# Performance work log

Measured on AMD Instinct MI355X. Metric: run time of the kernel, lower is better.

The kernel has to match this reference:

```python
import jax, jax.numpy as jnp
import numpy as np

D = 1024
H = 16
DK = D // H
FF = int(8 / 3 * D)  # 2730
EPS = 1e-6


def setup_inputs() -> dict:
    key = jax.random.key(0)
    ks = jax.random.split(key, 8)
    s = lambda n: 1.0 / np.sqrt(n)
    return {
        "x": jax.random.normal(ks[0], (2, 2048, D), dtype=jnp.float32),
        "w_qkv": jax.random.normal(ks[1], (3 * D, D), dtype=jnp.float32) * s(D),
        "w_o": jax.random.normal(ks[2], (D, D), dtype=jnp.float32) * s(D),
        "n1_w": jnp.ones((D,), dtype=jnp.float32),
        "n2_w": jnp.ones((D,), dtype=jnp.float32),
        "w1": jax.random.normal(ks[3], (FF, D), dtype=jnp.float32) * s(D),
        "w2": jax.random.normal(ks[4], (D, FF), dtype=jnp.float32) * s(FF),
        "w3": jax.random.normal(ks[5], (FF, D), dtype=jnp.float32) * s(D),
    }


def _rmsnorm(x, w):
    return x * jax.lax.rsqrt(jnp.mean(x * x, axis=-1, keepdims=True) + EPS) * w


def _attn(x, w_qkv, w_o):
    B, L, _ = x.shape
    qkv = x @ w_qkv.T                       # [B,L,3D]
    qkv = qkv.reshape(B, L, 3, H, DK)
    q, k, v = qkv[:, :, 0], qkv[:, :, 1], qkv[:, :, 2]   # [B,L,H,DK]
    scores = jnp.einsum("blhd,bmhd->bhlm", q, k) / np.sqrt(DK).astype(np.float32)
    attn = jax.nn.softmax(scores, axis=-1)               # [B,H,L,L]
    out = jnp.einsum("bhlm,bmhd->blhd", attn, v).reshape(B, L, D)
    return out @ w_o.T


def _swiglu(x, w1, w2, w3):
    return (jax.nn.silu(x @ w1.T) * (x @ w3.T)) @ w2.T


def reference(x, w_qkv, w_o, n1_w, n2_w, w1, w2, w3):
    x = x + _attn(_rmsnorm(x, n1_w), w_qkv, w_o)
    return x + _swiglu(_rmsnorm(x, n2_w), w1, w2, w3)
```

## Files before the change

kernel.cpp:

```cpp
#include <hip/hip_runtime.h>
#include <stdint.h>


#define LSEQ   2048
#define DMODEL 1024
#define NHEAD  16
#define NTOK   4096
#define FFR    2730
#define FFP    2816
#define FF2    5632

typedef short  short8  __attribute__((ext_vector_type(8)));
typedef float  floatx4 __attribute__((ext_vector_type(4)));

__device__ __forceinline__ uint16_t f2bf(float f) {
  uint32_t u = __builtin_bit_cast(uint32_t, f);
  u += 0x7FFFu + ((u >> 16) & 1u);
  return (uint16_t)(u >> 16);
}
__device__ __forceinline__ float bf2f(uint16_t s) {
  uint32_t u = ((uint32_t)s) << 16;
  return __builtin_bit_cast(float, u);
}
__device__ __forceinline__ void gl2lds16(const void* g, void* l) {
  __builtin_amdgcn_global_load_lds(
      (const __attribute__((address_space(1))) unsigned int*)g,
      (__attribute__((address_space(3))) unsigned int*)l, 16, 0, 0);
}

__global__ __launch_bounds__(256) void cvt_all_k(const float* __restrict__ wqkv,
                                                 const float* __restrict__ wo,
                                                 const float* __restrict__ w1,
                                                 const float* __restrict__ w3,
                                                 uint16_t* __restrict__ dst) {
  int g = blockIdx.x;
  int c = threadIdx.x * 4;
  const float* src = nullptr;
  if (g < 3072)       src = wqkv + (size_t)g * 1024;
  else if (g < 4096)  src = wo + (size_t)(g - 3072) * 1024;
  else {
    int r = g - 4096;
    int u = r >> 6, wi = r & 63;
    int srow = u * 32 + (wi & 31);
    if (srow < FFR) src = ((wi < 32) ? w1 : w3) + (size_t)srow * 1024;
  }
  float4 v = src ? *(const float4*)(src + c) : float4{0, 0, 0, 0};
  uint64_t pack =  (uint64_t)f2bf(v.x)        | ((uint64_t)f2bf(v.y) << 16)
                | ((uint64_t)f2bf(v.z) << 32) | ((uint64_t)f2bf(v.w) << 48);
  *(uint64_t*)(dst + (size_t)g * 1024 + c) = pack;
}

__global__ void cvt_pad_k(const float* __restrict__ src, uint16_t* __restrict__ dst,
                          int rows, int cols, int cols_p, long total) {
  long idx = (long)blockIdx.x * 256 + threadIdx.x;
  if (idx >= total) return;
  int r = (int)(idx / cols_p);
  int c = (int)(idx % cols_p);
  float v = (r < rows && c < cols) ? src[(size_t)r * cols + c] : 0.0f;
  dst[idx] = f2bf(v);
}

__global__ __launch_bounds__(256) void rmsnorm_k(const float* __restrict__ x,
                                                 const float* __restrict__ wgt,
                                                 uint16_t* __restrict__ out) {
  const int row = blockIdx.x;
  const int c = threadIdx.x * 4;
  const float* xr = x + (size_t)row * DMODEL;
  float4 v = *(const float4*)(xr + c);
  float ss = v.x * v.x + v.y * v.y + v.z * v.z + v.w * v.w;
#pragma unroll
  for (int off = 32; off >= 1; off >>= 1) ss += __shfl_down(ss, off, 64);
  __shared__ float red[4];
  if ((threadIdx.x & 63) == 0) red[threadIdx.x >> 6] = ss;
  __syncthreads();
  float tot = red[0] + red[1] + red[2] + red[3];
  float scale = rsqrtf(tot * (1.0f / DMODEL) + 1e-6f);
  float4 wv = *(const float4*)(wgt + c);
  uint64_t pack =  (uint64_t)f2bf(v.x * scale * wv.x)
                | ((uint64_t)f2bf(v.y * scale * wv.y) << 16)
                | ((uint64_t)f2bf(v.z * scale * wv.z) << 32)
                | ((uint64_t)f2bf(v.w * scale * wv.w) << 48);
  *(uint64_t*)(out + (size_t)row * DMODEL + c) = pack;
}

template <int MODE, int TM, int TN>
__global__ __launch_bounds__(256) void gemm_bt(const uint16_t* __restrict__ A,
                                               const uint16_t* __restrict__ B,
                                               uint16_t* __restrict__ Cb,
                                               float* __restrict__ Cf,
                                               const float* __restrict__ Res,
                                               int M, int N, int K) {
  constexpr int FI = TM / 32, FJ = TN / 32;
  constexpr int NIT = (TM + TN) / 64;
  __shared__ uint16_t As[TM * 32];
  __shared__ uint16_t Bs[TN * 32];
  const int tid = threadIdx.x;
  const int w = tid >> 6, lane = tid & 63;
  const int grp = lane >> 4, l16 = lane & 15;
  const int m0 = blockIdx.y * TM, n0 = blockIdx.x * TN;
  const int rw = (w >> 1) * (TM / 2), cw = (w & 1) * (TN / 2);

  floatx4 acc[FI][FJ] = {};

  const uint16_t* gp[NIT];
  uint16_t* lp[NIT];
#pragma unroll
  for (int i = 0; i < NIT; i++) {
    int c = i * 256 + tid;
    if (c < TM * 4) {
      gp[i] = A + (size_t)(m0 + (c >> 2)) * K + (c & 3) * 8;
      lp[i] = As + c * 8;
    } else {
      int c2 = c - TM * 4;
      gp[i] = B + (size_t)(n0 + (c2 >> 2)) * K + (c2 & 3) * 8;
      lp[i] = Bs + c2 * 8;
    }
  }

  for (int k0 = 0; k0 < K; k0 += 32) {
#pragma unroll
    for (int i = 0; i < NIT; i++) gl2lds16(gp[i] + k0, lp[i]);
    __syncthreads();
    short8 af[FI], bfr[FJ];
#pragma unroll
    for (int i = 0; i < FI; i++)
      af[i] = *(const short8*)(As + (rw + i * 16 + l16) * 32 + grp * 8);
#pragma unroll
    for (int j = 0; j < FJ; j++)
      bfr[j] = *(const short8*)(Bs + (cw + j * 16 + l16) * 32 + grp * 8);
#pragma unroll
    for (int i = 0; i < FI; i++)
#pragma unroll
      for (int j = 0; j < FJ; j++)
        acc[i][j] = __builtin_amdgcn_mfma_f32_16x16x32_bf16(af[i], bfr[j], acc[i][j], 0, 0, 0);
    __syncthreads();
  }

  if constexpr (MODE == 2) {
    const int half = N >> 1;
#pragma unroll
    for (int i = 0; i < FI; i++) {
      const int mrow = m0 + rw + i * 16 + grp * 4;
#pragma unroll
      for (int j = 0; j < 2; j++) {
        const int gcol = (n0 >> 1) + (cw >> 1) + j * 16 + l16;
#pragma unroll
        for (int r = 0; r < 4; r++) {
          float a = acc[i][j][r];
          float bv = acc[i][j + 2][r];
          float ex = __builtin_amdgcn_exp2f(-a * 1.4426950408889634f);
          float s = a * __builtin_amdgcn_rcpf(1.0f + ex);
          Cb[(size_t)(mrow + r) * half + gcol] = f2bf(s * bv);
        }
      }
    }
  } else {
#pragma unroll
    for (int i = 0; i < FI; i++) {
#pragma unroll
      for (int j = 0; j < FJ; j++) {
        const int mrow = m0 + rw + i * 16 + grp * 4;
        const int ncol = n0 + cw + j * 16 + l16;
#pragma unroll
        for (int r = 0; r < 4; r++) {
          size_t idx = (size_t)(mrow + r) * N + ncol;
          float v = acc[i][j][r];
          if (MODE == 0) Cb[idx] = f2bf(v);
          else           Cf[idx] = v + Res[idx];
        }
      }
    }
  }
}

__global__ __launch_bounds__(256) void attn_flash(const uint16_t* __restrict__ qkv,
                                                  uint16_t* __restrict__ outp) {
  const int tid = threadIdx.x;
  const int w = tid >> 6, lane = tid & 63;
  const int grp = lane >> 4, l16 = lane & 15;
  const int lin = blockIdx.x;
  const int xcd = lin & 7;
  const int slot = lin >> 3;
  const int pair = xcd * 4 + (slot >> 4);
  const int qc = slot & 15;
  const int h = pair & 15, b = pair >> 4;
  const int q0 = qc * 128;

  __shared__ uint16_t Qs[8192];
  __shared__ uint16_t Ks[2][4096];
  __shared__ uint16_t Vt[2][64 * 76];
  __shared__ uint16_t Ps[128 * 76];

  const size_t base = ((size_t)b * LSEQ) * 3072 + (size_t)h * 64;

#pragma unroll
  for (int i = 0; i < 4; i++) {
    int c = i * 256 + tid;
    int row = c >> 3, cc = (c & 7) ^ (row & 7);
    gl2lds16(qkv + base + (size_t)(q0 + row) * 3072 + cc * 8, Qs + c * 8);
  }
#pragma unroll
  for (int i = 0; i < 2; i++) {
    int c = i * 256 + tid;
    int row = c >> 3, cc = (c & 7) ^ (row & 7);
    gl2lds16(qkv + base + (size_t)row * 3072 + 1024 + cc * 8, Ks[0] + c * 8);
  }
#pragma unroll
  for (int i = 0; i < 2; i++) {
    int c = i * 256 + tid;
    int tt = c & 63, db = c >> 6;
    uint4 vv = *(const uint4*)(qkv + base + (size_t)tt * 3072 + 2048 + db * 8);
    uint32_t uu[4] = {vv.x, vv.y, vv.z, vv.w};
#pragma unroll
    for (int e = 0; e < 4; e++) {
      Vt[0][(db * 8 + e * 2 + 0) * 76 + tt] = (uint16_t)(uu[e] & 0xFFFFu);
      Vt[0][(db * 8 + e * 2 + 1) * 76 + tt] = (uint16_t)(uu[e] >> 16);
    }
  }
  __syncthreads();

  short8 aq[2][2];
#pragma unroll
  for (int fi = 0; fi < 2; fi++) {
    const int qrow = w * 32 + fi * 16 + l16;
#pragma unroll
    for (int kk = 0; kk < 2; kk++) {
      int cc = kk * 4 + grp;
      aq[fi][kk] = *(const short8*)(Qs + (qrow * 8 + (cc ^ (qrow & 7))) * 8);
    }
  }

  float lsum[2][4] = {};
  floatx4 o_acc[2][4] = {};
  const float C = 0.125f * 1.4426950408889634f;

  for (int kc = 0; kc < LSEQ / 64; kc++) {
    const int cur = kc & 1, nxt = cur ^ 1;
    const bool pre = (kc + 1 < LSEQ / 64);
    const int t1 = (kc + 1) * 64;
    uint4 vv[2];
    if (pre) {
#pragma unroll
      for (int i = 0; i < 2; i++) {
        int c = i * 256 + tid;
        int row = c >> 3, cc = (c & 7) ^ (row & 7);
        gl2lds16(qkv + base + (size_t)(t1 + row) * 3072 + 1024 + cc * 8, Ks[nxt] + c * 8);
      }
#pragma unroll
      for (int i = 0; i < 2; i++) {
        int c = i * 256 + tid;
        int tt = c & 63, db = c >> 6;
        vv[i] = *(const uint4*)(qkv + base + (size_t)(t1 + tt) * 3072 + 2048 + db * 8);
      }
    }

    floatx4 s_acc[2][4] = {};
#pragma unroll
    for (int j = 0; j < 4; j++) {
      const int krow = j * 16 + l16;
#pragma unroll
      for (int kk = 0; kk < 2; kk++) {
        int cc = kk * 4 + grp;
        short8 bk = *(const short8*)(Ks[cur] + (krow * 8 + (cc ^ (krow & 7))) * 8);
#pragma unroll
        for (int fi = 0; fi < 2; fi++)
          s_acc[fi][j] = __builtin_amdgcn_mfma_f32_16x16x32_bf16(aq[fi][kk], bk, s_acc[fi][j], 0, 0, 0);
      }
    }

#pragma unroll
    for (int fi = 0; fi < 2; fi++) {
      const int prow = w * 32 + fi * 16 + grp * 4;
#pragma unroll
      for (int j = 0; j < 4; j++)
#pragma unroll
        for (int r = 0; r < 4; r++) {
          float pv = __builtin_amdgcn_exp2f(s_acc[fi][j][r] * C);
          lsum[fi][r] += pv;
          Ps[(prow + r) * 76 + j * 16 + l16] = f2bf(pv);
        }
    }

#pragma unroll
    for (int kk = 0; kk < 2; kk++) {
      short8 ap0 = *(const short8*)(Ps + (w * 32 + l16) * 76 + kk * 32 + grp * 8);
      short8 ap1 = *(const short8*)(Ps + (w * 32 + 16 + l16) * 76 + kk * 32 + grp * 8);
#pragma unroll
      for (int jj = 0; jj < 4; jj++) {
        short8 bv = *(const short8*)(Vt[cur] + (jj * 16 + l16) * 76 + kk * 32 + grp * 8);
        o_acc[0][jj] = __builtin_amdgcn_mfma_f32_16x16x32_bf16(ap0, bv, o_acc[0][jj], 0, 0, 0);
        o_acc[1][jj] = __builtin_amdgcn_mfma_f32_16x16x32_bf16(ap1, bv, o_acc[1][jj], 0, 0, 0);
      }
    }

    if (pre) {
#pragma unroll
      for (int i = 0; i < 2; i++) {
        int c = i * 256 + tid;
        int tt = c & 63, db = c >> 6;
        uint32_t uu[4] = {vv[i].x, vv[i].y, vv[i].z, vv[i].w};
#pragma unroll
        for (int e = 0; e < 4; e++) {
          Vt[nxt][(db * 8 + e * 2 + 0) * 76 + tt] = (uint16_t)(uu[e] & 0xFFFFu);
          Vt[nxt][(db * 8 + e * 2 + 1) * 76 + tt] = (uint16_t)(uu[e] >> 16);
        }
      }
    }
    __syncthreads();
  }

#pragma unroll
  for (int off = 8; off >= 1; off >>= 1)
#pragma unroll
    for (int fi = 0; fi < 2; fi++)
#pragma unroll
      for (int r = 0; r < 4; r++) lsum[fi][r] += __shfl_xor(lsum[fi][r], off, 64);
#pragma unroll
  for (int fi = 0; fi < 2; fi++)
#pragma unroll
    for (int jj = 0; jj < 4; jj++)
#pragma unroll
      for (int r = 0; r < 4; r++) {
        int row = b * LSEQ + q0 + w * 32 + fi * 16 + grp * 4 + r;
        float o = o_acc[fi][jj][r] * __builtin_amdgcn_rcpf(lsum[fi][r]);
        outp[(size_t)row * DMODEL + h * 64 + jj * 16 + l16] = f2bf(o);
      }
}

extern "C" void kernel_launch(void* const* d_in, const int* in_sizes, int n_in,
                              void* d_out, int out_size, void* d_ws, size_t ws_size,
                              hipStream_t stream) {
  const float* x    = (const float*)d_in[0];
  const float* wqkv = (const float*)d_in[1];
  const float* wo   = (const float*)d_in[2];
  const float* n1w  = (const float*)d_in[3];
  const float* n2w  = (const float*)d_in[4];
  const float* w1   = (const float*)d_in[5];
  const float* w2   = (const float*)d_in[6];
  const float* w3   = (const float*)d_in[7];
  float* out = (float*)d_out;

  char* p = (char*)d_ws;
  uint16_t* wall  = (uint16_t*)p; p += (size_t)9728 * 1024 * 2;
  uint16_t* wqkvb = wall;
  uint16_t* wob   = wall + (size_t)3072 * 1024;
  uint16_t* w13b  = wall + (size_t)4096 * 1024;
  uint16_t* w2b   = (uint16_t*)p; p += (size_t)1024 * FFP * 2;
  uint16_t* h1    = (uint16_t*)p; p += (size_t)NTOK * DMODEL * 2;
  uint16_t* qkvb  = (uint16_t*)p; p += (size_t)NTOK * 3072 * 2;
  uint16_t* attno = (uint16_t*)p; p += (size_t)NTOK * DMODEL * 2;
  float*    x1    = (float*)p;    p += (size_t)NTOK * DMODEL * 4;
  uint16_t* h2    = (uint16_t*)p; p += (size_t)NTOK * DMODEL * 2;
  uint16_t* gbuf  = (uint16_t*)p; p += (size_t)NTOK * FFP * 2;

  cvt_all_k<<<9728, 256, 0, stream>>>(wqkv, wo, w1, w3, wall);
  cvt_pad_k<<<(1024 * FFP) / 256, 256, 0, stream>>>(w2, w2b, 1024, FFR, FFP, 1024L * FFP);

  rmsnorm_k<<<NTOK, 256, 0, stream>>>(x, n1w, h1);
  gemm_bt<0, 128, 128><<<dim3(3072 / 128, NTOK / 128), 256, 0, stream>>>(
      h1, wqkvb, qkvb, nullptr, nullptr, NTOK, 3072, 1024);
  attn_flash<<<512, 256, 0, stream>>>(qkvb, attno);
  gemm_bt<1, 128, 64><<<dim3(1024 / 64, NTOK / 128), 256, 0, stream>>>(
      attno, wob, nullptr, x1, x, NTOK, 1024, 1024);
  rmsnorm_k<<<NTOK, 256, 0, stream>>>(x1, n2w, h2);
  gemm_bt<2, 128, 128><<<dim3(FF2 / 128, NTOK / 128), 256, 0, stream>>>(
      h2, w13b, gbuf, nullptr, nullptr, NTOK, FF2, 1024);
  gemm_bt<1, 128, 64><<<dim3(1024 / 64, NTOK / 128), 256, 0, stream>>>(
      gbuf, w2b, nullptr, out, x1, NTOK, 1024, FFP);
}
```

Before: 390.7 us.

## Halve attention query tile, compute transposed scores, use packed bf16 conversion

The attention kernel now handles 64 query rows per block instead of 128 and launches 1024 blocks, so each wave owns 16 query rows. It computes S^T (K as the A operand) so each lane holds a contiguous row fragment of P and can write packed bf16 pairs. Q and P share one LDS buffer and the row-sum reduction goes through LDS, which cuts LDS use and should raise occupancy. The convert and rmsnorm kernels use the hardware v_cvt_pk_bf16_f32 instruction instead of software rounding. Smaller tiles mean K/V are read from global memory twice as often per query, and the padded strides change the LDS bank-conflict pattern.

```diff
diff --git a/kernel.cpp b/kernel.cpp
--- a/kernel.cpp
+++ b/kernel.cpp
@@ -10,6 +10,9 @@
 #define FFP    2816
 #define FF2    5632
 
+#define PSTR   72
+#define VSTR   70
+
 typedef short  short8  __attribute__((ext_vector_type(8)));
 typedef float  floatx4 __attribute__((ext_vector_type(4)));
 
@@ -21,6 +24,11 @@
 __device__ __forceinline__ float bf2f(uint16_t s) {
   uint32_t u = ((uint32_t)s) << 16;
   return __builtin_bit_cast(float, u);
+}
+__device__ __forceinline__ uint32_t pk_bf16(float a, float b) {
+  uint32_t d;
+  asm("v_cvt_pk_bf16_f32 %0, %1, %2" : "=v"(d) : "v"(a), "v"(b));
+  return d;
 }
 __device__ __forceinline__ void gl2lds16(const void* g, void* l) {
   __builtin_amdgcn_global_load_lds(
@@ -45,9 +53,8 @@
     if (srow < FFR) src = ((wi < 32) ? w1 : w3) + (size_t)srow * 1024;
   }
   float4 v = src ? *(const float4*)(src + c) : float4{0, 0, 0, 0};
-  uint64_t pack =  (uint64_t)f2bf(v.x)        | ((uint64_t)f2bf(v.y) << 16)
-                | ((uint64_t)f2bf(v.z) << 32) | ((uint64_t)f2bf(v.w) << 48);
-  *(uint64_t*)(dst + (size_t)g * 1024 + c) = pack;
+  uint2 pk = {pk_bf16(v.x, v.y), pk_bf16(v.z, v.w)};
+  *(uint2*)(dst + (size_t)g * 1024 + c) = pk;
 }
 
 __global__ void cvt_pad_k(const float* __restrict__ src, uint16_t* __restrict__ dst,
@@ -76,11 +83,9 @@
   float tot = red[0] + red[1] + red[2] + red[3];
   float scale = rsqrtf(tot * (1.0f / DMODEL) + 1e-6f);
   float4 wv = *(const float4*)(wgt + c);
-  uint64_t pack =  (uint64_t)f2bf(v.x * scale * wv.x)
-                | ((uint64_t)f2bf(v.y * scale * wv.y) << 16)
-                | ((uint64_t)f2bf(v.z * scale * wv.z) << 32)
-                | ((uint64_t)f2bf(v.w * scale * wv.w) << 48);
-  *(uint64_t*)(out + (size_t)row * DMODEL + c) = pack;
+  uint2 pk = {pk_bf16(v.x * scale * wv.x, v.y * scale * wv.y),
+              pk_bf16(v.z * scale * wv.z, v.w * scale * wv.w)};
+  *(uint2*)(out + (size_t)row * DMODEL + c) = pk;
 }
 
 template <int MODE, int TM, int TN>
@@ -181,20 +186,21 @@
   const int lin = blockIdx.x;
   const int xcd = lin & 7;
   const int slot = lin >> 3;
-  const int pair = xcd * 4 + (slot >> 4);
-  const int qc = slot & 15;
+  const int pair = xcd * 4 + (slot >> 5);
+  const int qc = slot & 31;
   const int h = pair & 15, b = pair >> 4;
-  const int q0 = qc * 128;
-
-  __shared__ uint16_t Qs[8192];
+  const int q0 = qc * 64;
+
+  __shared__ uint16_t QP[64 * PSTR];
   __shared__ uint16_t Ks[2][4096];
-  __shared__ uint16_t Vt[2][64 * 76];
-  __shared__ uint16_t Ps[128 * 76];
+  __shared__ uint16_t Vt[2][64 * VSTR];
+  uint16_t* Qs = QP;
+  uint16_t* Ps = QP;
 
   const size_t base = ((size_t)b * LSEQ) * 3072 + (size_t)h * 64;
 
 #pragma unroll
-  for (int i = 0; i < 4; i++) {
+  for (int i = 0; i < 2; i++) {
     int c = i * 256 + tid;
     int row = c >> 3, cc = (c & 7) ^ (row & 7);
     gl2lds16(qkv + base + (size_t)(q0 + row) * 3072 + cc * 8, Qs + c * 8);
@@ -213,25 +219,25 @@
     uint32_t uu[4] = {vv.x, vv.y, vv.z, vv.w};
 #pragma unroll
     for (int e = 0; e < 4; e++) {
-      Vt[0][(db * 8 + e * 2 + 0) * 76 + tt] = (uint16_t)(uu[e] & 0xFFFFu);
-      Vt[0][(db * 8 + e * 2 + 1) * 76 + tt] = (uint16_t)(uu[e] >> 16);
+      Vt[0][(db * 8 + e * 2 + 0) * VSTR + tt] = (uint16_t)(uu[e] & 0xFFFFu);
+      Vt[0][(db * 8 + e * 2 + 1) * VSTR + tt] = (uint16_t)(uu[e] >> 16);
     }
   }
   __syncthreads();
 
-  short8 aq[2][2];
-#pragma unroll
-  for (int fi = 0; fi < 2; fi++) {
-    const int qrow = w * 32 + fi * 16 + l16;
+  short8 aq[2];
+  {
+    const int qrow = w * 16 + l16;
 #pragma unroll
     for (int kk = 0; kk < 2; kk++) {
       int cc = kk * 4 + grp;
-      aq[fi][kk] = *(const short8*)(Qs + (qrow * 8 + (cc ^ (qrow & 7))) * 8);
-    }
-  }
-
-  float lsum[2][4] = {};
-  floatx4 o_acc[2][4] = {};
+      aq[kk] = *(const short8*)(Qs + (qrow * 8 + (cc ^ (qrow & 7))) * 8);
+    }
+  }
+  __syncthreads();
+
+  float lsum = 0.0f;
+  floatx4 o_acc[4] = {};
   const float C = 0.125f * 1.4426950408889634f;
 
   for (int kc = 0; kc < LSEQ / 64; kc++) {
@@ -254,42 +260,39 @@
       }
     }
 
-    floatx4 s_acc[2][4] = {};
-#pragma unroll
-    for (int j = 0; j < 4; j++) {
-      const int krow = j * 16 + l16;
+    floatx4 s_acc[4] = {};
+#pragma unroll
+    for (int jm = 0; jm < 4; jm++) {
+      const int krow = jm * 16 + l16;
 #pragma unroll
       for (int kk = 0; kk < 2; kk++) {
         int cc = kk * 4 + grp;
-        short8 bk = *(const short8*)(Ks[cur] + (krow * 8 + (cc ^ (krow & 7))) * 8);
-#pragma unroll
-        for (int fi = 0; fi < 2; fi++)
-          s_acc[fi][j] = __builtin_amdgcn_mfma_f32_16x16x32_bf16(aq[fi][kk], bk, s_acc[fi][j], 0, 0, 0);
-      }
-    }
-
-#pragma unroll
-    for (int fi = 0; fi < 2; fi++) {
-      const int prow = w * 32 + fi * 16 + grp * 4;
-#pragma unroll
-      for (int j = 0; j < 4; j++)
-#pragma unroll
-        for (int r = 0; r < 4; r++) {
-          float pv = __builtin_amdgcn_exp2f(s_acc[fi][j][r] * C);
-          lsum[fi][r] += pv;
-          Ps[(prow + r) * 76 + j * 16 + l16] = f2bf(pv);
-        }
+        short8 ak = *(const short8*)(Ks[cur] + (krow * 8 + (cc ^ (krow & 7))) * 8);
+        s_acc[jm] = __builtin_amdgcn_mfma_f32_16x16x32_bf16(ak, aq[kk], s_acc[jm], 0, 0, 0);
+      }
+    }
+
+    {
+      uint16_t* prow = Ps + (w * 16 + l16) * PSTR;
+#pragma unroll
+      for (int jm = 0; jm < 4; jm++) {
+        float p0 = __builtin_amdgcn_exp2f(s_acc[jm][0] * C);
+        float p1 = __builtin_amdgcn_exp2f(s_acc[jm][1] * C);
+        float p2 = __builtin_amdgcn_exp2f(s_acc[jm][2] * C);
+        float p3 = __builtin_amdgcn_exp2f(s_acc[jm][3] * C);
+        lsum += (p0 + p1) + (p2 + p3);
+        uint2 pk = {pk_bf16(p0, p1), pk_bf16(p2, p3)};
+        *(uint2*)(prow + jm * 16 + grp * 4) = pk;
+      }
     }
 
 #pragma unroll
     for (int kk = 0; kk < 2; kk++) {
-      short8 ap0 = *(const short8*)(Ps + (w * 32 + l16) * 76 + kk * 32 + grp * 8);
-      short8 ap1 = *(const short8*)(Ps + (w * 32 + 16 + l16) * 76 + kk * 32 + grp * 8);
-#pragma unroll
-      for (int jj = 0; jj < 4; jj++) {
-        short8 bv = *(const short8*)(Vt[cur] + (jj * 16 + l16) * 76 + kk * 32 + grp * 8);
-        o_acc[0][jj] = __builtin_amdgcn_mfma_f32_16x16x32_bf16(ap0, bv, o_acc[0][jj], 0, 0, 0);
-        o_acc[1][jj] = __builtin_amdgcn_mfma_f32_16x16x32_bf16(ap1, bv, o_acc[1][jj], 0, 0, 0);
+      short8 ap = *(const short8*)(Ps + (w * 16 + l16) * PSTR + kk * 32 + grp * 8);
+#pragma unroll
+      for (int jd = 0; jd < 4; jd++) {
+        short8 bv = *(const short8*)(Vt[cur] + (jd * 16 + l16) * VSTR + kk * 32 + grp * 8);
+        o_acc[jd] = __builtin_amdgcn_mfma_f32_16x16x32_bf16(ap, bv, o_acc[jd], 0, 0, 0);
       }
     }
 
@@ -301,30 +304,29 @@
         uint32_t uu[4] = {vv[i].x, vv[i].y, vv[i].z, vv[i].w};
 #pragma unroll
         for (int e = 0; e < 4; e++) {
-          Vt[nxt][(db * 8 + e * 2 + 0) * 76 + tt] = (uint16_t)(uu[e] & 0xFFFFu);
-          Vt[nxt][(db * 8 + e * 2 + 1) * 76 + tt] = (uint16_t)(uu[e] >> 16);
+          Vt[nxt][(db * 8 + e * 2 + 0) * VSTR + tt] = (uint16_t)(uu[e] & 0xFFFFu);
+          Vt[nxt][(db * 8 + e * 2 + 1) * VSTR + tt] = (uint16_t)(uu[e] >> 16);
         }
       }
     }
     __syncthreads();
   }
 
-#pragma unroll
-  for (int off = 8; off >= 1; off >>= 1)
-#pragma unroll
-    for (int fi = 0; fi < 2; fi++)
-#pragma unroll
-      for (int r = 0; r < 4; r++) lsum[fi][r] += __shfl_xor(lsum[fi][r], off, 64);
-#pragma unroll
-  for (int fi = 0; fi < 2; fi++)
-#pragma unroll
-    for (int jj = 0; jj < 4; jj++)
-#pragma unroll
-      for (int r = 0; r < 4; r++) {
-        int row = b * LSEQ + q0 + w * 32 + fi * 16 + grp * 4 + r;
-        float o = o_acc[fi][jj][r] * __builtin_amdgcn_rcpf(lsum[fi][r]);
-        outp[(size_t)row * DMODEL + h * 64 + jj * 16 + l16] = f2bf(o);
-      }
+  lsum += __shfl_xor(lsum, 16, 64);
+  lsum += __shfl_xor(lsum, 32, 64);
+  float* Ls = (float*)Ks[0];
+  if (grp == 0) Ls[w * 16 + l16] = lsum;
+  __syncthreads();
+  float rq[4];
+#pragma unroll
+  for (int r = 0; r < 4; r++) rq[r] = __builtin_amdgcn_rcpf(Ls[w * 16 + grp * 4 + r]);
+#pragma unroll
+  for (int jd = 0; jd < 4; jd++)
+#pragma unroll
+    for (int r = 0; r < 4; r++) {
+      int row = b * LSEQ + q0 + w * 16 + grp * 4 + r;
+      outp[(size_t)row * DMODEL + h * 64 + jd * 16 + l16] = f2bf(o_acc[jd][r] * rq[r]);
+    }
 }
 
 extern "C" void kernel_launch(void* const* d_in, const int* in_sizes, int n_in,
@@ -359,7 +361,7 @@
   rmsnorm_k<<<NTOK, 256, 0, stream>>>(x, n1w, h1);
   gemm_bt<0, 128, 128><<<dim3(3072 / 128, NTOK / 128), 256, 0, stream>>>(
       h1, wqkvb, qkvb, nullptr, nullptr, NTOK, 3072, 1024);
-  attn_flash<<<512, 256, 0, stream>>>(qkvb, attno);
+  attn_flash<<<1024, 256, 0, stream>>>(qkvb, attno);
   gemm_bt<1, 128, 64><<<dim3(1024 / 64, NTOK / 128), 256, 0, stream>>>(
       attno, wob, nullptr, x1, x, NTOK, 1024, 1024);
   rmsnorm_k<<<NTOK, 256, 0, stream>>>(x1, n2w, h2);
```

Result: slower. 409.9 us (+4.9%).
